# Kernel tuning notes

Measured on AMD Instinct MI355X. Metric: run time of the kernel, lower is better.

Reference implementation:

```python
import jax, jax.numpy as jnp
import numpy as np

N_HEADS = 16

def setup_inputs() -> dict:
    key = jax.random.key(0)
    k1, k2, k3, k4 = jax.random.split(key, 4)
    B, S, H = 2, 2048, 1024
    x = jax.random.normal(k1, (B, S, H), dtype=jnp.float32)
    pos_table = jax.random.normal(k2, (S, H), dtype=jnp.float32) * 0.02
    W_qkv = jax.random.normal(k3, (H, 3 * H), dtype=jnp.float32) * (1.0 / np.sqrt(H))
    W_out = jax.random.normal(k4, (H, H), dtype=jnp.float32) * (1.0 / np.sqrt(H))
    return {"x": x, "pos_table": pos_table, "W_qkv": W_qkv, "W_out": W_out}


def reference(x, pos_table, W_qkv, W_out):
    B, S, Hd = x.shape
    nh = N_HEADS
    hs = Hd // nh  # head_size
    NEG_INF = jnp.float32(-10000.0)

    pos = pos_table[:S][None, :, :]  # [1, S, H]
    # q, k come from (x + pos_emb); v comes from x alone (duplicate projection)
    qk_proj = (x + pos) @ W_qkv              # [B, S, 3H]
    q = qk_proj[..., :Hd]
    k = qk_proj[..., Hd:2 * Hd]
    v = x @ W_qkv[:, 2 * Hd:]                # [B, S, H]

    def split_heads(t):  # [B, S, H] -> [B, nh, S, hs]
        return t.reshape(B, S, nh, hs).transpose(0, 2, 1, 3)

    q, k, v = split_heads(q), split_heads(k), split_heads(v)

    scores = jnp.einsum('bhqd,bhkd->bhqk', q, k) / jnp.sqrt(jnp.float32(hs))
    q_ind = jnp.arange(S)[:, None]
    k_ind = jnp.arange(S)[None, :]
    mask = q_ind < k_ind  # True where future (masked)
    scores = jnp.where(mask, NEG_INF, scores)

    probs = jax.nn.softmax(scores, axis=-1)
    out = jnp.einsum('bhqk,bhkd->bhqd', probs, v)  # [B, nh, S, hs]
    out = out.transpose(0, 2, 1, 3).reshape(B, S, Hd)
    return out @ W_out
```

## Files before the change

kernel.cpp:

```cpp
#include <hip/hip_runtime.h>

#define SEQ     2048
#define HDIM    1024
#define TOKENS  4096
#define NHEADS  16
#define HS      64
#define LP      72
#define LPS     72

typedef __bf16 v8bf __attribute__((ext_vector_type(8)));
typedef float  v4f  __attribute__((ext_vector_type(4)));

#define MFMA16(a, b, c) __builtin_amdgcn_mfma_f32_16x16x32_bf16((a), (b), (c), 0, 0, 0)

#define QSCALE (0.125f * 1.44269504088896f)

__device__ __forceinline__ unsigned short f2bf(float f) {
  unsigned int u = __float_as_uint(f);
  u += 0x7FFFu + ((u >> 16) & 1u);
  return (unsigned short)(u >> 16);
}
__device__ __forceinline__ float bf2f(unsigned short u) {
  return __uint_as_float((unsigned int)u << 16);
}

__device__ __forceinline__ void async16(const void* g, void* l) {
  __builtin_amdgcn_global_load_lds(
      (const __attribute__((address_space(1))) void*)g,
      (__attribute__((address_space(3))) void*)l, 16, 0, 0);
}

__global__ __launch_bounds__(256) void prep_x_kernel(
    const float* __restrict__ x, const float* __restrict__ pos,
    unsigned short* __restrict__ X, unsigned short* __restrict__ XP) {
  const int i = (blockIdx.x * 256 + threadIdx.x) * 4;
  float4 xv = *(const float4*)(x + i);
  float4 pv = *(const float4*)(pos + (i & (SEQ * HDIM - 1)));
  ushort4 a, b;
  a.x = f2bf(xv.x); a.y = f2bf(xv.y); a.z = f2bf(xv.z); a.w = f2bf(xv.w);
  b.x = f2bf(xv.x + pv.x); b.y = f2bf(xv.y + pv.y);
  b.z = f2bf(xv.z + pv.z); b.w = f2bf(xv.w + pv.w);
  *(ushort4*)(X + i) = a;
  *(ushort4*)(XP + i) = b;
}

__global__ __launch_bounds__(256) void transpose_kernel(
    const float* __restrict__ in, unsigned short* __restrict__ out, int R, int C) {
  __shared__ float tile[32][33];
  const int bx = blockIdx.x * 32, by = blockIdx.y * 32;
  const int tx = threadIdx.x & 31, ty = threadIdx.x >> 5;
#pragma unroll
  for (int j = 0; j < 32; j += 8)
    tile[ty + j][tx] = in[(size_t)(by + ty + j) * C + bx + tx];
  __syncthreads();
#pragma unroll
  for (int j = 0; j < 32; j += 8)
    out[(size_t)(bx + ty + j) * R + by + tx] = f2bf(tile[tx][ty + j]);
}

__global__ __launch_bounds__(256) void gemm_qkv_kernel(
    const unsigned short* __restrict__ XP, const unsigned short* __restrict__ X,
    const unsigned short* __restrict__ Wt,
    unsigned short* __restrict__ Qb, unsigned short* __restrict__ Kb,
    unsigned short* __restrict__ VTb) {
  __shared__ unsigned short As[128 * 32];
  __shared__ unsigned short Bs[128 * 32];
  const int m0 = blockIdx.x * 128;
  const int n0 = blockIdx.y * 128;
  const unsigned short* A = (n0 < 2 * HDIM) ? XP : X;
  const int t = threadIdx.x;
  const int lane = t & 63, w = t >> 6;
  const int wm = (w >> 1) * 64, wn = (w & 1) * 64;
  const int quad = lane >> 4, l15 = lane & 15;

  v4f acc[4][4] = {};

  const int rowA = t >> 2;
  const int colA = (t & 3) * 8;
  const unsigned short* gA = A + (size_t)(m0 + rowA) * HDIM + colA;
  const unsigned short* gB = Wt + (size_t)(n0 + rowA) * HDIM + colA;
  unsigned short* lA = &As[t * 8];
  unsigned short* lB = &Bs[t * 8];

  for (int k0 = 0; k0 < HDIM; k0 += 32) {
    __syncthreads();
    async16(gA + k0, lA);
    async16(gA + 64 * HDIM + k0, lA + 64 * 32);
    async16(gB + k0, lB);
    async16(gB + 64 * HDIM + k0, lB + 64 * 32);
    __syncthreads();
    v8bf a[4], b[4];
#pragma unroll
    for (int i = 0; i < 4; i++)
      a[i] = *(const v8bf*)&As[(wm + i * 16 + l15) * 32 + quad * 8];
#pragma unroll
    for (int i = 0; i < 4; i++)
      b[i] = *(const v8bf*)&Bs[(wn + i * 16 + l15) * 32 + quad * 8];
#pragma unroll
    for (int i = 0; i < 4; i++)
#pragma unroll
      for (int j = 0; j < 4; j++)
        acc[i][j] = MFMA16(a[i], b[j], acc[i][j]);
  }

#pragma unroll
  for (int i = 0; i < 4; i++) {
#pragma unroll
    for (int j = 0; j < 4; j++) {
#pragma unroll
      for (int r = 0; r < 4; r++) {
        const int tr = m0 + wm + i * 16 + quad * 4 + r;
        const int c = n0 + wn + j * 16 + l15;
        const int b_ = tr >> 11;
        const int s_ = tr & (SEQ - 1);
        const float val = acc[i][j][r];
        if (c < HDIM) {
          const int h = c >> 6, d = c & 63;
          Qb[((size_t)((b_ << 4) | h) * SEQ + s_) * HS + d] = f2bf(val * QSCALE);
        } else if (c < 2 * HDIM) {
          const int c2 = c - HDIM;
          const int h = c2 >> 6, d = c2 & 63;
          Kb[((size_t)((b_ << 4) | h) * SEQ + s_) * HS + d] = f2bf(val);
        } else {
          const int c2 = c - 2 * HDIM;
          const int h = c2 >> 6, d = c2 & 63;
          VTb[((size_t)((b_ << 4) | h) * HS + d) * SEQ + s_] = f2bf(val);
        }
      }
    }
  }
}

__global__ __launch_bounds__(256, 4) void attn_kernel(
    const unsigned short* __restrict__ Qp, const unsigned short* __restrict__ Kp,
    const unsigned short* __restrict__ Vp, unsigned short* __restrict__ ATTN,
    unsigned short* __restrict__ PART_O, float* __restrict__ PART_L) {
  __shared__ unsigned short Qs[64 * LP];
  __shared__ unsigned short Ks[64 * LP];
  __shared__ unsigned short Vs[64 * LP];
  __shared__ unsigned short Ps[4][16 * LPS];

  const int L = blockIdx.x;
  int qblk, seg;
  if (L < 8)       { qblk = L;                 seg = 0; }
  else if (L < 24) { qblk = 8  + ((L - 8) >> 1);  seg = (L - 8) & 1; }
  else if (L < 48) { qblk = 16 + (L - 24) / 3;    seg = (L - 24) % 3; }
  else             { qblk = 24 + ((L - 48) >> 2); seg = (L - 48) & 3; }

  const int bh = blockIdx.y;
  const int b_ = bh >> 4, h = bh & 15;
  const int q0 = qblk * 64;
  const int t = threadIdx.x;
  const int lane = t & 63, w = t >> 6;
  const int quad = lane >> 4, l15 = lane & 15;

  const unsigned short* Qg = Qp + (size_t)bh * SEQ * HS;
  const unsigned short* Kg = Kp + (size_t)bh * SEQ * HS;
  const unsigned short* Vg = Vp + (size_t)bh * HS * SEQ;

  const int sr = t >> 3, scol = (t & 7) * 8;
  {
    *(uint4*)&Qs[sr * LP + scol] = *(const uint4*)(Qg + (size_t)(q0 + sr) * HS + scol);
    *(uint4*)&Qs[(sr + 32) * LP + scol] =
        *(const uint4*)(Qg + (size_t)(q0 + sr + 32) * HS + scol);
  }
  __syncthreads();
  const v8bf bq0 = *(const v8bf*)&Qs[(w * 16 + l15) * LP + quad * 8];
  const v8bf bq1 = *(const v8bf*)&Qs[(w * 16 + l15) * LP + 32 + quad * 8];

  v8bf ones;
#pragma unroll
  for (int j = 0; j < 8; j++) ones[j] = (__bf16)1.0f;

  v4f o[4] = {};
  v4f lacc = {};

  const int c_lo = seg * 8;
  const int c_hi = min(c_lo + 8, qblk + 1);

  uint4 kr0, kr1, vr0, vr1;
  {
    const int kc = c_lo * 64;
    kr0 = *(const uint4*)(Kg + (size_t)(kc + sr) * HS + scol);
    kr1 = *(const uint4*)(Kg + (size_t)(kc + sr + 32) * HS + scol);
    vr0 = *(const uint4*)(Vg + (size_t)sr * SEQ + kc + scol);
    vr1 = *(const uint4*)(Vg + (size_t)(sr + 32) * SEQ + kc + scol);
  }

  const int qrow_l = q0 + w * 16 + l15;
  for (int cI = c_lo; cI < c_hi; cI++) {
    const int kc = cI * 64;
    __syncthreads();
    *(uint4*)&Ks[sr * LP + scol] = kr0;
    *(uint4*)&Ks[(sr + 32) * LP + scol] = kr1;
    *(uint4*)&Vs[sr * LP + scol] = vr0;
    *(uint4*)&Vs[(sr + 32) * LP + scol] = vr1;
    if (cI + 1 < c_hi) {
      const int kn = kc + 64;
      kr0 = *(const uint4*)(Kg + (size_t)(kn + sr) * HS + scol);
      kr1 = *(const uint4*)(Kg + (size_t)(kn + sr + 32) * HS + scol);
      vr0 = *(const uint4*)(Vg + (size_t)sr * SEQ + kn + scol);
      vr1 = *(const uint4*)(Vg + (size_t)(sr + 32) * SEQ + kn + scol);
    }
    __syncthreads();

    v4f sc[4] = {};
#pragma unroll
    for (int ni = 0; ni < 4; ni++) {
      v8bf k0 = *(const v8bf*)&Ks[(ni * 16 + l15) * LP + quad * 8];
      v8bf k1 = *(const v8bf*)&Ks[(ni * 16 + l15) * LP + 32 + quad * 8];
      sc[ni] = MFMA16(k0, bq0, sc[ni]);
      sc[ni] = MFMA16(k1, bq1, sc[ni]);
    }

    if (cI == qblk) {
#pragma unroll
      for (int ni = 0; ni < 4; ni++) {
        const int key = kc + ni * 16 + quad * 4;
#pragma unroll
        for (int r = 0; r < 4; r++)
          if (key + r > qrow_l) sc[ni][r] = -1e30f;
      }
    }

#pragma unroll
    for (int ni = 0; ni < 4; ni++) {
      const float p0 = exp2f(sc[ni][0]), p1 = exp2f(sc[ni][1]);
      const float p2 = exp2f(sc[ni][2]), p3 = exp2f(sc[ni][3]);
      uint2 pk;
      pk.x = __builtin_amdgcn_perm(__float_as_uint(p1), __float_as_uint(p0), 0x07060302u);
      pk.y = __builtin_amdgcn_perm(__float_as_uint(p3), __float_as_uint(p2), 0x07060302u);
      *(uint2*)&Ps[w][l15 * LPS + ni * 16 + quad * 4] = pk;
    }

#pragma unroll
    for (int ki = 0; ki < 2; ki++) {
      v8bf pa = *(const v8bf*)&Ps[w][l15 * LPS + ki * 32 + quad * 8];
      lacc = MFMA16(pa, ones, lacc);
#pragma unroll
      for (int ni = 0; ni < 4; ni++) {
        v8bf vb = *(const v8bf*)&Vs[(ni * 16 + l15) * LP + ki * 32 + quad * 8];
        o[ni] = MFMA16(pa, vb, o[ni]);
      }
    }
  }

  const int row_base = q0 + w * 16 + quad * 4;
  if (qblk < 8) {
    float invl[4];
#pragma unroll
    for (int r = 0; r < 4; r++) invl[r] = 1.0f / lacc[r];
#pragma unroll
    for (int ni = 0; ni < 4; ni++)
#pragma unroll
      for (int r = 0; r < 4; r++) {
        const int tr = b_ * SEQ + row_base + r;
        ATTN[(size_t)tr * HDIM + h * HS + ni * 16 + l15] = f2bf(o[ni][r] * invl[r]);
      }
  } else {
    const int off_q = (qblk < 16) ? (qblk - 8) * 2
                    : (qblk < 24) ? 16 + (qblk - 16) * 3
                                  : 40 + (qblk - 24) * 4;
    const int slot = bh * 72 + off_q + seg;
    unsigned short* po = PART_O + (size_t)slot * 4096;
#pragma unroll
    for (int ni = 0; ni < 4; ni++)
#pragma unroll
      for (int r = 0; r < 4; r++)
        po[(w * 16 + quad * 4 + r) * 64 + ni * 16 + l15] = f2bf(o[ni][r]);
    if (l15 == 0) {
      float* pl = PART_L + (size_t)slot * 128;
#pragma unroll
      for (int r = 0; r < 4; r++) pl[w * 16 + quad * 4 + r] = lacc[r];
    }
  }
}

__global__ __launch_bounds__(256) void combine_kernel(
    const unsigned short* __restrict__ PART_O, const float* __restrict__ PART_L,
    unsigned short* __restrict__ ATTN) {
  const int qblk = 8 + blockIdx.x;
  const int bh = blockIdx.y;
  const int b_ = bh >> 4, h = bh & 15;
  const int nseg = (qblk >> 3) + 1;
  const int off_q = (qblk < 16) ? (qblk - 8) * 2
                  : (qblk < 24) ? 16 + (qblk - 16) * 3
                                : 40 + (qblk - 24) * 4;
  const int slot0 = bh * 72 + off_q;
  const int t = threadIdx.x;
  const int row = t >> 2, c0 = (t & 3) * 16;

  float Lsum = 0.0f;
  for (int s = 0; s < nseg; s++)
    Lsum += PART_L[(size_t)(slot0 + s) * 128 + row];
  const float inv = 1.0f / Lsum;

  float acc[16];
#pragma unroll
  for (int j = 0; j < 16; j++) acc[j] = 0.0f;
  for (int s = 0; s < nseg; s++) {
    const unsigned short* po = PART_O + (size_t)(slot0 + s) * 4096 + row * 64 + c0;
    ushort4 u0 = *(const ushort4*)(po);
    ushort4 u1 = *(const ushort4*)(po + 4);
    ushort4 u2 = *(const ushort4*)(po + 8);
    ushort4 u3 = *(const ushort4*)(po + 12);
    acc[0]  += bf2f(u0.x); acc[1]  += bf2f(u0.y);
    acc[2]  += bf2f(u0.z); acc[3]  += bf2f(u0.w);
    acc[4]  += bf2f(u1.x); acc[5]  += bf2f(u1.y);
    acc[6]  += bf2f(u1.z); acc[7]  += bf2f(u1.w);
    acc[8]  += bf2f(u2.x); acc[9]  += bf2f(u2.y);
    acc[10] += bf2f(u2.z); acc[11] += bf2f(u2.w);
    acc[12] += bf2f(u3.x); acc[13] += bf2f(u3.y);
    acc[14] += bf2f(u3.z); acc[15] += bf2f(u3.w);
  }

  const int tr = b_ * SEQ + qblk * 64 + row;
  unsigned short* dst = ATTN + (size_t)tr * HDIM + h * HS + c0;
  ushort4 o0, o1, o2, o3;
  o0.x = f2bf(acc[0] * inv);  o0.y = f2bf(acc[1] * inv);
  o0.z = f2bf(acc[2] * inv);  o0.w = f2bf(acc[3] * inv);
  o1.x = f2bf(acc[4] * inv);  o1.y = f2bf(acc[5] * inv);
  o1.z = f2bf(acc[6] * inv);  o1.w = f2bf(acc[7] * inv);
  o2.x = f2bf(acc[8] * inv);  o2.y = f2bf(acc[9] * inv);
  o2.z = f2bf(acc[10] * inv); o2.w = f2bf(acc[11] * inv);
  o3.x = f2bf(acc[12] * inv); o3.y = f2bf(acc[13] * inv);
  o3.z = f2bf(acc[14] * inv); o3.w = f2bf(acc[15] * inv);
  *(ushort4*)(dst) = o0;
  *(ushort4*)(dst + 4) = o1;
  *(ushort4*)(dst + 8) = o2;
  *(ushort4*)(dst + 12) = o3;
}

__global__ __launch_bounds__(256) void gemm_out_kernel(
    const unsigned short* __restrict__ Ab, const unsigned short* __restrict__ Wt,
    float* __restrict__ out) {
  __shared__ unsigned short As[128 * 32];
  __shared__ unsigned short Bs[128 * 32];
  const int m0 = blockIdx.x * 128;
  const int n0 = blockIdx.y * 128;
  const int t = threadIdx.x;
  const int lane = t & 63, w = t >> 6;
  const int wm = (w >> 1) * 64, wn = (w & 1) * 64;
  const int quad = lane >> 4, l15 = lane & 15;

  v4f acc[4][4] = {};

  const int rowA = t >> 2;
  const int colA = (t & 3) * 8;
  const unsigned short* gA = Ab + (size_t)(m0 + rowA) * HDIM + colA;
  const unsigned short* gB = Wt + (size_t)(n0 + rowA) * HDIM + colA;
  unsigned short* lA = &As[t * 8];
  unsigned short* lB = &Bs[t * 8];

  for (int k0 = 0; k0 < HDIM; k0 += 32) {
    __syncthreads();
    async16(gA + k0, lA);
    async16(gA + 64 * HDIM + k0, lA + 64 * 32);
    async16(gB + k0, lB);
    async16(gB + 64 * HDIM + k0, lB + 64 * 32);
    __syncthreads();
    v8bf a[4], b[4];
#pragma unroll
    for (int i = 0; i < 4; i++)
      a[i] = *(const v8bf*)&As[(wm + i * 16 + l15) * 32 + quad * 8];
#pragma unroll
    for (int i = 0; i < 4; i++)
      b[i] = *(const v8bf*)&Bs[(wn + i * 16 + l15) * 32 + quad * 8];
#pragma unroll
    for (int i = 0; i < 4; i++)
#pragma unroll
      for (int j = 0; j < 4; j++)
        acc[i][j] = MFMA16(a[i], b[j], acc[i][j]);
  }

#pragma unroll
  for (int i = 0; i < 4; i++) {
#pragma unroll
    for (int j = 0; j < 4; j++) {
#pragma unroll
      for (int r = 0; r < 4; r++) {
        const int tr = m0 + wm + i * 16 + quad * 4 + r;
        const int c = n0 + wn + j * 16 + l15;
        out[(size_t)tr * HDIM + c] = acc[i][j][r];
      }
    }
  }
}

extern "C" void kernel_launch(void* const* d_in, const int* in_sizes, int n_in,
                              void* d_out, int out_size, void* d_ws, size_t ws_size,
                              hipStream_t stream) {
  (void)in_sizes; (void)n_in; (void)out_size; (void)ws_size;
  const float* x    = (const float*)d_in[0];
  const float* pos  = (const float*)d_in[1];
  const float* Wqkv = (const float*)d_in[2];
  const float* Wout = (const float*)d_in[3];
  float* out = (float*)d_out;

  char* ws = (char*)d_ws;
  unsigned short* XP   = (unsigned short*)(ws);
  unsigned short* X    = (unsigned short*)(ws + ((size_t)8  << 20));
  unsigned short* WQT  = (unsigned short*)(ws + ((size_t)16 << 20));
  unsigned short* WOT  = (unsigned short*)(ws + ((size_t)22 << 20));
  unsigned short* Qb   = (unsigned short*)(ws + ((size_t)24 << 20));
  unsigned short* Kb   = (unsigned short*)(ws + ((size_t)32 << 20));
  unsigned short* VTb  = (unsigned short*)(ws + ((size_t)40 << 20));
  unsigned short* ATTN = (unsigned short*)(ws + ((size_t)48 << 20));
  unsigned short* PART_O = (unsigned short*)(ws);
  float*          PART_L = (float*)(ws + ((size_t)19 << 20));

  prep_x_kernel<<<TOKENS * HDIM / 1024, 256, 0, stream>>>(x, pos, X, XP);

  dim3 gt1(3 * HDIM / 32, HDIM / 32);
  transpose_kernel<<<gt1, 256, 0, stream>>>(Wqkv, WQT, HDIM, 3 * HDIM);
  dim3 gt2(HDIM / 32, HDIM / 32);
  transpose_kernel<<<gt2, 256, 0, stream>>>(Wout, WOT, HDIM, HDIM);

  dim3 g1(TOKENS / 128, 3 * HDIM / 128);
  gemm_qkv_kernel<<<g1, 256, 0, stream>>>(XP, X, WQT, Qb, Kb, VTb);

  dim3 g2(80, 2 * NHEADS);
  attn_kernel<<<g2, 256, 0, stream>>>(Qb, Kb, VTb, ATTN, PART_O, PART_L);

  dim3 gc(24, 2 * NHEADS);
  combine_kernel<<<gc, 256, 0, stream>>>(PART_O, PART_L, ATTN);

  dim3 g3(TOKENS / 128, HDIM / 128);
  gemm_out_kernel<<<g3, 256, 0, stream>>>(ATTN, WOT, out);
}
```

Before: 202.7 us.

## Use 128-row query tiles in attention and stage QKV epilogue through LDS

The attention kernel now handles 128 query rows per block, two 16-row fragments per wave, so each K/V tile loaded into LDS is reused across twice as many queries. This halves the grid, the split-K partial slots and the combine work, at the cost of more registers and fewer blocks. The QKV GEMM epilogue now writes the tile into a padded LDS buffer and then issues coalesced 16-byte stores for Q, K and transposed V, replacing scattered 2-byte stores. The added ~34KB of LDS may lower occupancy of the GEMM.

```diff
diff --git a/kernel.cpp b/kernel.cpp
--- a/kernel.cpp
+++ b/kernel.cpp
@@ -6,7 +6,6 @@
 #define NHEADS  16
 #define HS      64
 #define LP      72
-#define LPS     72
 
 typedef __bf16 v8bf __attribute__((ext_vector_type(8)));
 typedef float  v4f  __attribute__((ext_vector_type(4)));
@@ -65,6 +64,7 @@
     unsigned short* __restrict__ VTb) {
   __shared__ unsigned short As[128 * 32];
   __shared__ unsigned short Bs[128 * 32];
+  __shared__ unsigned short St[128 * 136];
   const int m0 = blockIdx.x * 128;
   const int n0 = blockIdx.y * 128;
   const unsigned short* A = (n0 < 2 * HDIM) ? XP : X;
@@ -103,53 +103,73 @@
         acc[i][j] = MFMA16(a[i], b[j], acc[i][j]);
   }
 
-#pragma unroll
-  for (int i = 0; i < 4; i++) {
-#pragma unroll
-    for (int j = 0; j < 4; j++) {
-#pragma unroll
-      for (int r = 0; r < 4; r++) {
-        const int tr = m0 + wm + i * 16 + quad * 4 + r;
-        const int c = n0 + wn + j * 16 + l15;
-        const int b_ = tr >> 11;
-        const int s_ = tr & (SEQ - 1);
-        const float val = acc[i][j][r];
-        if (c < HDIM) {
-          const int h = c >> 6, d = c & 63;
-          Qb[((size_t)((b_ << 4) | h) * SEQ + s_) * HS + d] = f2bf(val * QSCALE);
-        } else if (c < 2 * HDIM) {
-          const int c2 = c - HDIM;
-          const int h = c2 >> 6, d = c2 & 63;
-          Kb[((size_t)((b_ << 4) | h) * SEQ + s_) * HS + d] = f2bf(val);
-        } else {
-          const int c2 = c - 2 * HDIM;
-          const int h = c2 >> 6, d = c2 & 63;
-          VTb[((size_t)((b_ << 4) | h) * HS + d) * SEQ + s_] = f2bf(val);
-        }
-      }
-    }
-  }
-}
-
-__global__ __launch_bounds__(256, 4) void attn_kernel(
+  const int b_ = m0 >> 11;
+  const int s0 = m0 & (SEQ - 1);
+
+  if (n0 >= 2 * HDIM) {
+#pragma unroll
+    for (int i = 0; i < 4; i++)
+#pragma unroll
+      for (int j = 0; j < 4; j++) {
+        ushort4 u;
+        u.x = f2bf(acc[i][j][0]); u.y = f2bf(acc[i][j][1]);
+        u.z = f2bf(acc[i][j][2]); u.w = f2bf(acc[i][j][3]);
+        *(ushort4*)&St[(wn + j * 16 + l15) * 136 + wm + i * 16 + quad * 4] = u;
+      }
+    __syncthreads();
+#pragma unroll
+    for (int it = 0; it < 8; it++) {
+      const int lin = it * 256 + t;
+      const int n = lin >> 4, s8 = (lin & 15) * 8;
+      const int c2 = (n0 - 2 * HDIM) + n;
+      const int h = c2 >> 6, d = c2 & 63;
+      *(uint4*)(VTb + ((size_t)(((b_ << 4) | h) * HS + d)) * SEQ + s0 + s8) =
+          *(const uint4*)&St[n * 136 + s8];
+    }
+  } else {
+    const float scale = (n0 < HDIM) ? QSCALE : 1.0f;
+#pragma unroll
+    for (int i = 0; i < 4; i++)
+#pragma unroll
+      for (int j = 0; j < 4; j++)
+#pragma unroll
+        for (int r = 0; r < 4; r++)
+          St[(wm + i * 16 + quad * 4 + r) * 136 + wn + j * 16 + l15] =
+              f2bf(acc[i][j][r] * scale);
+    __syncthreads();
+    unsigned short* dst = (n0 < HDIM) ? Qb : Kb;
+    const int c2base = n0 & (HDIM - 1);
+#pragma unroll
+    for (int it = 0; it < 8; it++) {
+      const int lin = it * 256 + t;
+      const int m = lin >> 4, d8 = (lin & 15) * 8;
+      const int c2 = c2base + d8;
+      const int h = c2 >> 6, d = c2 & 63;
+      *(uint4*)(dst + ((size_t)(((b_ << 4) | h) * SEQ + s0 + m)) * HS + d) =
+          *(const uint4*)&St[m * 136 + d8];
+    }
+  }
+}
+
+__global__ __launch_bounds__(256) void attn_kernel(
     const unsigned short* __restrict__ Qp, const unsigned short* __restrict__ Kp,
     const unsigned short* __restrict__ Vp, unsigned short* __restrict__ ATTN,
     unsigned short* __restrict__ PART_O, float* __restrict__ PART_L) {
-  __shared__ unsigned short Qs[64 * LP];
+  __shared__ unsigned short Qs[128 * LP];
   __shared__ unsigned short Ks[64 * LP];
   __shared__ unsigned short Vs[64 * LP];
-  __shared__ unsigned short Ps[4][16 * LPS];
+  __shared__ unsigned short Ps[4][32 * LP];
 
   const int L = blockIdx.x;
   int qblk, seg;
-  if (L < 8)       { qblk = L;                 seg = 0; }
-  else if (L < 24) { qblk = 8  + ((L - 8) >> 1);  seg = (L - 8) & 1; }
-  else if (L < 48) { qblk = 16 + (L - 24) / 3;    seg = (L - 24) % 3; }
-  else             { qblk = 24 + ((L - 48) >> 2); seg = (L - 48) & 3; }
+  if (L < 4)       { qblk = L;                  seg = 0; }
+  else if (L < 12) { qblk = 4  + ((L - 4) >> 1);  seg = (L - 4) & 1; }
+  else if (L < 24) { qblk = 8  + (L - 12) / 3;    seg = (L - 12) % 3; }
+  else             { qblk = 12 + ((L - 24) >> 2); seg = (L - 24) & 3; }
 
   const int bh = blockIdx.y;
   const int b_ = bh >> 4, h = bh & 15;
-  const int q0 = qblk * 64;
+  const int q0 = qblk * 128;
   const int t = threadIdx.x;
   const int lane = t & 63, w = t >> 6;
   const int quad = lane >> 4, l15 = lane & 15;
@@ -159,24 +179,27 @@
   const unsigned short* Vg = Vp + (size_t)bh * HS * SEQ;
 
   const int sr = t >> 3, scol = (t & 7) * 8;
-  {
-    *(uint4*)&Qs[sr * LP + scol] = *(const uint4*)(Qg + (size_t)(q0 + sr) * HS + scol);
-    *(uint4*)&Qs[(sr + 32) * LP + scol] =
-        *(const uint4*)(Qg + (size_t)(q0 + sr + 32) * HS + scol);
-  }
+#pragma unroll
+  for (int i = 0; i < 4; i++)
+    *(uint4*)&Qs[(sr + i * 32) * LP + scol] =
+        *(const uint4*)(Qg + (size_t)(q0 + sr + i * 32) * HS + scol);
   __syncthreads();
-  const v8bf bq0 = *(const v8bf*)&Qs[(w * 16 + l15) * LP + quad * 8];
-  const v8bf bq1 = *(const v8bf*)&Qs[(w * 16 + l15) * LP + 32 + quad * 8];
+  v8bf bq[2][2];
+#pragma unroll
+  for (int qf = 0; qf < 2; qf++)
+#pragma unroll
+    for (int kh = 0; kh < 2; kh++)
+      bq[qf][kh] = *(const v8bf*)&Qs[(w * 32 + qf * 16 + l15) * LP + kh * 32 + quad * 8];
 
   v8bf ones;
 #pragma unroll
   for (int j = 0; j < 8; j++) ones[j] = (__bf16)1.0f;
 
-  v4f o[4] = {};
-  v4f lacc = {};
+  v4f o[2][4] = {};
+  v4f lacc[2] = {};
 
   const int c_lo = seg * 8;
-  const int c_hi = min(c_lo + 8, qblk + 1);
+  const int c_hi = min(c_lo + 8, 2 * qblk + 2);
 
   uint4 kr0, kr1, vr0, vr1;
   {
@@ -187,7 +210,6 @@
     vr1 = *(const uint4*)(Vg + (size_t)(sr + 32) * SEQ + kc + scol);
   }
 
-  const int qrow_l = q0 + w * 16 + l15;
   for (int cI = c_lo; cI < c_hi; cI++) {
     const int kc = cI * 64;
     __syncthreads();
@@ -204,74 +226,94 @@
     }
     __syncthreads();
 
-    v4f sc[4] = {};
+    v8bf kf[4][2];
 #pragma unroll
     for (int ni = 0; ni < 4; ni++) {
-      v8bf k0 = *(const v8bf*)&Ks[(ni * 16 + l15) * LP + quad * 8];
-      v8bf k1 = *(const v8bf*)&Ks[(ni * 16 + l15) * LP + 32 + quad * 8];
-      sc[ni] = MFMA16(k0, bq0, sc[ni]);
-      sc[ni] = MFMA16(k1, bq1, sc[ni]);
-    }
-
-    if (cI == qblk) {
+      kf[ni][0] = *(const v8bf*)&Ks[(ni * 16 + l15) * LP + quad * 8];
+      kf[ni][1] = *(const v8bf*)&Ks[(ni * 16 + l15) * LP + 32 + quad * 8];
+    }
+
+    const bool diag = (cI >= 2 * qblk);
+#pragma unroll
+    for (int qf = 0; qf < 2; qf++) {
+      v4f sc[4] = {};
 #pragma unroll
       for (int ni = 0; ni < 4; ni++) {
-        const int key = kc + ni * 16 + quad * 4;
-#pragma unroll
-        for (int r = 0; r < 4; r++)
-          if (key + r > qrow_l) sc[ni][r] = -1e30f;
-      }
-    }
-
-#pragma unroll
-    for (int ni = 0; ni < 4; ni++) {
-      const float p0 = exp2f(sc[ni][0]), p1 = exp2f(sc[ni][1]);
-      const float p2 = exp2f(sc[ni][2]), p3 = exp2f(sc[ni][3]);
-      uint2 pk;
-      pk.x = __builtin_amdgcn_perm(__float_as_uint(p1), __float_as_uint(p0), 0x07060302u);
-      pk.y = __builtin_amdgcn_perm(__float_as_uint(p3), __float_as_uint(p2), 0x07060302u);
-      *(uint2*)&Ps[w][l15 * LPS + ni * 16 + quad * 4] = pk;
+        sc[ni] = MFMA16(kf[ni][0], bq[qf][0], sc[ni]);
+        sc[ni] = MFMA16(kf[ni][1], bq[qf][1], sc[ni]);
+      }
+      if (diag) {
+        const int qrow = q0 + w * 32 + qf * 16 + l15;
+#pragma unroll
+        for (int ni = 0; ni < 4; ni++) {
+          const int key = kc + ni * 16 + quad * 4;
+#pragma unroll
+          for (int r = 0; r < 4; r++)
+            if (key + r > qrow) sc[ni][r] = -1e30f;
+        }
+      }
+#pragma unroll
+      for (int ni = 0; ni < 4; ni++) {
+        const float p0 = exp2f(sc[ni][0]), p1 = exp2f(sc[ni][1]);
+        const float p2 = exp2f(sc[ni][2]), p3 = exp2f(sc[ni][3]);
+        uint2 pk;
+        pk.x = __builtin_amdgcn_perm(__float_as_uint(p1), __float_as_uint(p0), 0x07060302u);
+        pk.y = __builtin_amdgcn_perm(__float_as_uint(p3), __float_as_uint(p2), 0x07060302u);
+        *(uint2*)&Ps[w][(qf * 16 + l15) * LP + ni * 16 + quad * 4] = pk;
+      }
     }
 
 #pragma unroll
     for (int ki = 0; ki < 2; ki++) {
-      v8bf pa = *(const v8bf*)&Ps[w][l15 * LPS + ki * 32 + quad * 8];
-      lacc = MFMA16(pa, ones, lacc);
+      v8bf pa[2];
+#pragma unroll
+      for (int qf = 0; qf < 2; qf++) {
+        pa[qf] = *(const v8bf*)&Ps[w][(qf * 16 + l15) * LP + ki * 32 + quad * 8];
+        lacc[qf] = MFMA16(pa[qf], ones, lacc[qf]);
+      }
 #pragma unroll
       for (int ni = 0; ni < 4; ni++) {
         v8bf vb = *(const v8bf*)&Vs[(ni * 16 + l15) * LP + ki * 32 + quad * 8];
-        o[ni] = MFMA16(pa, vb, o[ni]);
-      }
-    }
-  }
-
-  const int row_base = q0 + w * 16 + quad * 4;
-  if (qblk < 8) {
-    float invl[4];
-#pragma unroll
-    for (int r = 0; r < 4; r++) invl[r] = 1.0f / lacc[r];
-#pragma unroll
-    for (int ni = 0; ni < 4; ni++)
-#pragma unroll
-      for (int r = 0; r < 4; r++) {
-        const int tr = b_ * SEQ + row_base + r;
-        ATTN[(size_t)tr * HDIM + h * HS + ni * 16 + l15] = f2bf(o[ni][r] * invl[r]);
-      }
+#pragma unroll
+        for (int qf = 0; qf < 2; qf++)
+          o[qf][ni] = MFMA16(pa[qf], vb, o[qf][ni]);
+      }
+    }
+  }
+
+  if (qblk < 4) {
+#pragma unroll
+    for (int qf = 0; qf < 2; qf++) {
+      const int row_base = q0 + w * 32 + qf * 16 + quad * 4;
+      float invl[4];
+#pragma unroll
+      for (int r = 0; r < 4; r++) invl[r] = 1.0f / lacc[qf][r];
+#pragma unroll
+      for (int ni = 0; ni < 4; ni++)
+#pragma unroll
+        for (int r = 0; r < 4; r++) {
+          const int tr = b_ * SEQ + row_base + r;
+          ATTN[(size_t)tr * HDIM + h * HS + ni * 16 + l15] = f2bf(o[qf][ni][r] * invl[r]);
+        }
+    }
   } else {
-    const int off_q = (qblk < 16) ? (qblk - 8) * 2
-                    : (qblk < 24) ? 16 + (qblk - 16) * 3
-                                  : 40 + (qblk - 24) * 4;
-    const int slot = bh * 72 + off_q + seg;
-    unsigned short* po = PART_O + (size_t)slot * 4096;
-#pragma unroll
-    for (int ni = 0; ni < 4; ni++)
-#pragma unroll
-      for (int r = 0; r < 4; r++)
-        po[(w * 16 + quad * 4 + r) * 64 + ni * 16 + l15] = f2bf(o[ni][r]);
-    if (l15 == 0) {
-      float* pl = PART_L + (size_t)slot * 128;
-#pragma unroll
-      for (int r = 0; r < 4; r++) pl[w * 16 + quad * 4 + r] = lacc[r];
+    const int off_q = (qblk < 8)  ? (qblk - 4) * 2
+                    : (qblk < 12) ? 8 + (qblk - 8) * 3
+                                  : 20 + (qblk - 12) * 4;
+    const int slot = bh * 36 + off_q + seg;
+    unsigned short* po = PART_O + (size_t)slot * 8192;
+    float* pl = PART_L + (size_t)slot * 128;
+#pragma unroll
+    for (int qf = 0; qf < 2; qf++) {
+      const int rb = w * 32 + qf * 16 + quad * 4;
+#pragma unroll
+      for (int ni = 0; ni < 4; ni++)
+#pragma unroll
+        for (int r = 0; r < 4; r++)
+          po[(rb + r) * 64 + ni * 16 + l15] = f2bf(o[qf][ni][r]);
+      if (l15 == 0)
+#pragma unroll
+        for (int r = 0; r < 4; r++) pl[rb + r] = lacc[qf][r];
     }
   }
 }
@@ -279,56 +321,60 @@
 __global__ __launch_bounds__(256) void combine_kernel(
     const unsigned short* __restrict__ PART_O, const float* __restrict__ PART_L,
     unsigned short* __restrict__ ATTN) {
-  const int qblk = 8 + blockIdx.x;
+  const int qblk = 4 + blockIdx.x;
   const int bh = blockIdx.y;
   const int b_ = bh >> 4, h = bh & 15;
-  const int nseg = (qblk >> 3) + 1;
-  const int off_q = (qblk < 16) ? (qblk - 8) * 2
-                  : (qblk < 24) ? 16 + (qblk - 16) * 3
-                                : 40 + (qblk - 24) * 4;
-  const int slot0 = bh * 72 + off_q;
+  const int nseg = (qblk >> 2) + 1;
+  const int off_q = (qblk < 8)  ? (qblk - 4) * 2
+                  : (qblk < 12) ? 8 + (qblk - 8) * 3
+                                : 20 + (qblk - 12) * 4;
+  const int slot0 = bh * 36 + off_q;
   const int t = threadIdx.x;
-  const int row = t >> 2, c0 = (t & 3) * 16;
-
-  float Lsum = 0.0f;
-  for (int s = 0; s < nseg; s++)
-    Lsum += PART_L[(size_t)(slot0 + s) * 128 + row];
-  const float inv = 1.0f / Lsum;
-
-  float acc[16];
-#pragma unroll
-  for (int j = 0; j < 16; j++) acc[j] = 0.0f;
-  for (int s = 0; s < nseg; s++) {
-    const unsigned short* po = PART_O + (size_t)(slot0 + s) * 4096 + row * 64 + c0;
-    ushort4 u0 = *(const ushort4*)(po);
-    ushort4 u1 = *(const ushort4*)(po + 4);
-    ushort4 u2 = *(const ushort4*)(po + 8);
-    ushort4 u3 = *(const ushort4*)(po + 12);
-    acc[0]  += bf2f(u0.x); acc[1]  += bf2f(u0.y);
-    acc[2]  += bf2f(u0.z); acc[3]  += bf2f(u0.w);
-    acc[4]  += bf2f(u1.x); acc[5]  += bf2f(u1.y);
-    acc[6]  += bf2f(u1.z); acc[7]  += bf2f(u1.w);
-    acc[8]  += bf2f(u2.x); acc[9]  += bf2f(u2.y);
-    acc[10] += bf2f(u2.z); acc[11] += bf2f(u2.w);
-    acc[12] += bf2f(u3.x); acc[13] += bf2f(u3.y);
-    acc[14] += bf2f(u3.z); acc[15] += bf2f(u3.w);
-  }
-
-  const int tr = b_ * SEQ + qblk * 64 + row;
-  unsigned short* dst = ATTN + (size_t)tr * HDIM + h * HS + c0;
-  ushort4 o0, o1, o2, o3;
-  o0.x = f2bf(acc[0] * inv);  o0.y = f2bf(acc[1] * inv);
-  o0.z = f2bf(acc[2] * inv);  o0.w = f2bf(acc[3] * inv);
-  o1.x = f2bf(acc[4] * inv);  o1.y = f2bf(acc[5] * inv);
-  o1.z = f2bf(acc[6] * inv);  o1.w = f2bf(acc[7] * inv);
-  o2.x = f2bf(acc[8] * inv);  o2.y = f2bf(acc[9] * inv);
-  o2.z = f2bf(acc[10] * inv); o2.w = f2bf(acc[11] * inv);
-  o3.x = f2bf(acc[12] * inv); o3.y = f2bf(acc[13] * inv);
-  o3.z = f2bf(acc[14] * inv); o3.w = f2bf(acc[15] * inv);
-  *(ushort4*)(dst) = o0;
-  *(ushort4*)(dst + 4) = o1;
-  *(ushort4*)(dst + 8) = o2;
-  *(ushort4*)(dst + 12) = o3;
+
+#pragma unroll
+  for (int rr = 0; rr < 2; rr++) {
+    const int row = rr * 64 + (t >> 2), c0 = (t & 3) * 16;
+
+    float Lsum = 0.0f;
+    for (int s = 0; s < nseg; s++)
+      Lsum += PART_L[(size_t)(slot0 + s) * 128 + row];
+    const float inv = 1.0f / Lsum;
+
+    float acc[16];
+#pragma unroll
+    for (int j = 0; j < 16; j++) acc[j] = 0.0f;
+    for (int s = 0; s < nseg; s++) {
+      const unsigned short* po = PART_O + (size_t)(slot0 + s) * 8192 + row * 64 + c0;
+      ushort4 u0 = *(const ushort4*)(po);
+      ushort4 u1 = *(const ushort4*)(po + 4);
+      ushort4 u2 = *(const ushort4*)(po + 8);
+      ushort4 u3 = *(const ushort4*)(po + 12);
+      acc[0]  += bf2f(u0.x); acc[1]  += bf2f(u0.y);
+      acc[2]  += bf2f(u0.z); acc[3]  += bf2f(u0.w);
+      acc[4]  += bf2f(u1.x); acc[5]  += bf2f(u1.y);
+      acc[6]  += bf2f(u1.z); acc[7]  += bf2f(u1.w);
+      acc[8]  += bf2f(u2.x); acc[9]  += bf2f(u2.y);
+      acc[10] += bf2f(u2.z); acc[11] += bf2f(u2.w);
+      acc[12] += bf2f(u3.x); acc[13] += bf2f(u3.y);
+      acc[14] += bf2f(u3.z); acc[15] += bf2f(u3.w);
+    }
+
+    const int tr = b_ * SEQ + qblk * 128 + row;
+    unsigned short* dst = ATTN + (size_t)tr * HDIM + h * HS + c0;
+    ushort4 o0, o1, o2, o3;
+    o0.x = f2bf(acc[0] * inv);  o0.y = f2bf(acc[1] * inv);
+    o0.z = f2bf(acc[2] * inv);  o0.w = f2bf(acc[3] * inv);
+    o1.x = f2bf(acc[4] * inv);  o1.y = f2bf(acc[5] * inv);
+    o1.z = f2bf(acc[6] * inv);  o1.w = f2bf(acc[7] * inv);
+    o2.x = f2bf(acc[8] * inv);  o2.y = f2bf(acc[9] * inv);
+    o2.z = f2bf(acc[10] * inv); o2.w = f2bf(acc[11] * inv);
+    o3.x = f2bf(acc[12] * inv); o3.y = f2bf(acc[13] * inv);
+    o3.z = f2bf(acc[14] * inv); o3.w = f2bf(acc[15] * inv);
+    *(ushort4*)(dst) = o0;
+    *(ushort4*)(dst + 4) = o1;
+    *(ushort4*)(dst + 8) = o2;
+    *(ushort4*)(dst + 12) = o3;
+  }
 }
 
 __global__ __launch_bounds__(256) void gemm_out_kernel(
@@ -419,10 +465,10 @@
   dim3 g1(TOKENS / 128, 3 * HDIM / 128);
   gemm_qkv_kernel<<<g1, 256, 0, stream>>>(XP, X, WQT, Qb, Kb, VTb);
 
-  dim3 g2(80, 2 * NHEADS);
+  dim3 g2(40, 2 * NHEADS);
   attn_kernel<<<g2, 256, 0, stream>>>(Qb, Kb, VTb, ATTN, PART_O, PART_L);
 
-  dim3 gc(24, 2 * NHEADS);
+  dim3 gc(12, 2 * NHEADS);
   combine_kernel<<<gc, 256, 0, stream>>>(PART_O, PART_L, ATTN);
 
   dim3 g3(TOKENS / 128, HDIM / 128);
```

Result: slower. 213.6 us (+5.3%).
